# Kernel optimization log

Measured on AMD Instinct MI355X. Metric: run time of the kernel, lower is better.

Reference implementation:

```python
import jax, jax.numpy as jnp
import numpy as np

N = 50000       # nodes
E = 800000      # edges
IN = 64         # input node feature dim
H = 4           # attention heads
C = 32          # per-head channels (h_dim)
HC = H * C      # 128, concat output per conv
ED = 16         # edge feature dim
G = 2000        # number of graphs (molecules)
NEG = 0.2       # GATConv negative slope


def setup_inputs() -> dict:
    key = jax.random.key(0)
    ks = jax.random.split(key, 40)
    rn = lambda k, shp, s=0.1: (jax.random.normal(k, shp, jnp.float32) * s)
    inp = {}
    inp["x"] = jax.random.normal(ks[0], (N, IN), jnp.float32)
    inp["edge_index"] = jax.random.randint(ks[1], (2, E), 0, N)
    inp["edge_attr"] = jax.random.normal(ks[2], (E, ED), jnp.float32)
    inp["batch"] = jnp.sort(jax.random.randint(ks[3], (N,), 0, G))
    dins = [IN, HC, HC]
    i = 4
    for l in (1, 2, 3):
        din = dins[l - 1]
        inp[f"W{l}"] = rn(ks[i], (din, HC)); i += 1
        inp[f"as{l}"] = rn(ks[i], (H, C)); i += 1
        inp[f"ad{l}"] = rn(ks[i], (H, C)); i += 1
        inp[f"We{l}"] = rn(ks[i], (ED, HC)); i += 1
        inp[f"ae{l}"] = rn(ks[i], (H, C)); i += 1
        inp[f"b{l}"] = rn(ks[i], (HC,)); i += 1
    D = 4 * HC
    inp["lw1"] = rn(ks[i], (D, D)); i += 1
    inp["lb1"] = rn(ks[i], (D,)); i += 1
    inp["lw2"] = rn(ks[i], (D, 1)); i += 1
    inp["lb2"] = rn(ks[i], (1,)); i += 1
    return inp


def gat_conv(x, src, dst, edge_attr, W, a_s, a_d, We, a_e, b):
    n = x.shape[0]
    h = (x @ W).reshape(n, H, C)                       # [N,H,C]
    alpha_src = (h * a_s).sum(-1)                      # [N,H]
    alpha_dst = (h * a_d).sum(-1)                      # [N,H]
    he = (edge_attr @ We).reshape(-1, H, C)            # [E,H,C]
    alpha_edge = (he * a_e).sum(-1)                    # [E,H]
    alpha = jax.nn.leaky_relu(alpha_src[src] + alpha_dst[dst] + alpha_edge, NEG)
    # per-destination softmax over incoming edges (stable)
    amax = jax.ops.segment_max(alpha, dst, num_segments=n)
    amax = jnp.where(jnp.isfinite(amax), amax, 0.0)
    ex = jnp.exp(alpha - amax[dst])                    # [E,H]
    denom = jax.ops.segment_sum(ex, dst, num_segments=n)
    w = ex / (denom[dst] + 1e-16)                      # [E,H]
    m = h[src] * w[:, :, None]                         # [E,H,C]
    out = jax.ops.segment_sum(m, dst, num_segments=n)  # [N,H,C]
    return out.reshape(n, HC) + b


def reference(x, edge_index, edge_attr, batch,
              W1, as1, ad1, We1, ae1, b1,
              W2, as2, ad2, We2, ae2, b2,
              W3, as3, ad3, We3, ae3, b3,
              lw1, lb1, lw2, lb2):
    src, dst = edge_index[0], edge_index[1]
    h1 = gat_conv(x, src, dst, edge_attr, W1, as1, ad1, We1, ae1, b1)
    h2 = gat_conv(h1, src, dst, edge_attr, W2, as2, ad2, We2, ae2, b2)
    h3 = gat_conv(h2, src, dst, edge_attr, W3, as3, ad3, We3, ae3, b3)
    h_pool = jax.ops.segment_sum(h3, batch, num_segments=G)  # global_add_pool
    h_pool_ = h_pool[batch]                                  # == repeat_interleave by counts
    h = jnp.concatenate([h1, h2, h3, h_pool_], axis=1)       # [N, 4*HC]
    h = jax.nn.leaky_relu(h @ lw1 + lb1, 0.01)               # torch LeakyReLU default
    return h @ lw2 + lb2                                     # [N, 1]
```

## Files before the change

kernel.cpp:

```cpp
#include <hip/hip_runtime.h>
#include <hip/hip_bf16.h>
#include <math.h>

#define NN 50000
#define NE 800000
#define DIN1 64
#define NHEAD 4
#define CH 32
#define HC 128
#define EDIM 16
#define NG 2000
#define SP 56
#define MAXCH 64
#define MJ 256

typedef __attribute__((ext_vector_type(8))) short short8;
typedef __attribute__((ext_vector_type(4))) float floatx4;

__device__ __forceinline__ float lrelu(float x, float s) { return x > 0.f ? x : s * x; }

__device__ __forceinline__ unsigned short f2bf(float x) {
  unsigned int u = __float_as_uint(x);
  u += 0x7fff + ((u >> 16) & 1);
  return (unsigned short)(u >> 16);
}
__device__ __forceinline__ float bflo(unsigned int u) { return __uint_as_float(u << 16); }
__device__ __forceinline__ float bfhi(unsigned int u) { return __uint_as_float(u & 0xffff0000u); }

__device__ __forceinline__ void async16(void* lds, const void* g) {
  __builtin_amdgcn_global_load_lds((const __attribute__((address_space(1))) unsigned int*)g,
                                   (__attribute__((address_space(3))) unsigned int*)lds, 16, 0, 0);
}

__global__ __launch_bounds__(256) void k_we_a(
    const float* __restrict__ We1, const float* __restrict__ ae1,
    const float* __restrict__ We2, const float* __restrict__ ae2,
    const float* __restrict__ We3, const float* __restrict__ ae3,
    float* __restrict__ we_a) {
  int t = threadIdx.x;
  if (t >= 3 * EDIM * NHEAD) return;
  int l = t / (EDIM * NHEAD);
  int rem = t % (EDIM * NHEAD);
  int d = rem / NHEAD, h = rem % NHEAD;
  const float* We = (l == 0) ? We1 : ((l == 1) ? We2 : We3);
  const float* ae = (l == 0) ? ae1 : ((l == 1) ? ae2 : ae3);
  float s = 0.f;
  for (int c = 0; c < CH; ++c) s += We[d * HC + h * CH + c] * ae[h * CH + c];
  we_a[t] = s;
}

__global__ __launch_bounds__(256) void k_wsd(
    const float* __restrict__ W1, const float* __restrict__ as1, const float* __restrict__ ad1,
    const float* __restrict__ W2, const float* __restrict__ as2, const float* __restrict__ ad2,
    const float* __restrict__ W3, const float* __restrict__ as3, const float* __restrict__ ad3,
    unsigned short* __restrict__ wsdb) {
  int i = blockIdx.x * 256 + threadIdx.x;
  if (i >= 3 * 16 * 128) return;
  int l = i >> 11;
  int col = (i >> 7) & 15;
  int k = i & 127;
  if (col >= 8 || (l == 0 && k >= DIN1)) { wsdb[i] = 0; return; }
  const float* W = (l == 0) ? W1 : ((l == 1) ? W2 : W3);
  int head = col & 3;
  const float* av = (col < 4) ? ((l == 0) ? as1 : ((l == 1) ? as2 : as3))
                              : ((l == 0) ? ad1 : ((l == 1) ? ad2 : ad3));
  float s = 0.f;
  for (int c = 0; c < CH; ++c) s += W[(size_t)k * HC + head * CH + c] * av[head * CH + c];
  wsdb[i] = f2bf(s);
}

__global__ __launch_bounds__(256) void k_lw1t(const float* __restrict__ lw1, unsigned short* __restrict__ lw1tb) {
  int i = blockIdx.x * 256 + threadIdx.x;
  if (i >= 512 * 384) return;
  int n = i / 384, k = i % 384;
  lw1tb[i] = f2bf(lw1[(size_t)k * 512 + n]);
}

__global__ __launch_bounds__(256) void k_wt(const float* __restrict__ W1, const float* __restrict__ W2,
                                            const float* __restrict__ W3, unsigned short* __restrict__ wtb) {
  int i = blockIdx.x * 256 + threadIdx.x;
  if (i < 128 * 64) {
    int j = i / 64, k = i % 64;
    wtb[i] = f2bf(W1[k * HC + j]);
  } else if (i < 128 * 64 + 128 * 128) {
    int ii = i - 128 * 64;
    int j = ii / 128, k = ii % 128;
    wtb[i] = f2bf(W2[k * HC + j]);
  } else if (i < 128 * 64 + 2 * 128 * 128) {
    int ii = i - (128 * 64 + 128 * 128);
    int j = ii / 128, k = ii % 128;
    wtb[i] = f2bf(W3[k * HC + j]);
  }
}

__global__ __launch_bounds__(256) void k_cast(const float* __restrict__ x, unsigned short* __restrict__ xb0) {
  int i = blockIdx.x * 256 + threadIdx.x;
  if (i < NN * DIN1) xb0[i] = f2bf(x[i]);
}

__global__ __launch_bounds__(256) void k_hist(const int* __restrict__ dst, int* __restrict__ cnt) {
  int e = blockIdx.x * 256 + threadIdx.x;
  if (e < NE) atomicAdd(&cnt[dst[e]], 1);
}

__global__ __launch_bounds__(256) void k_scan1(const int* __restrict__ cnt, int* __restrict__ row_start,
                                               int* __restrict__ aux) {
  __shared__ int s[256];
  int t = threadIdx.x;
  int i = blockIdx.x * 256 + t;
  int v = (i < NN) ? cnt[i] : 0;
  s[t] = v;
  __syncthreads();
  for (int off = 1; off < 256; off <<= 1) {
    int tv = (t >= off) ? s[t - off] : 0;
    __syncthreads();
    s[t] += tv;
    __syncthreads();
  }
  if (i < NN) row_start[i] = s[t] - v;
  if (t == 255) aux[blockIdx.x] = s[255];
}

__global__ __launch_bounds__(256) void k_scan2(int* __restrict__ aux, int nb) {
  __shared__ int s[256];
  int t = threadIdx.x;
  int v = (t < nb) ? aux[t] : 0;
  s[t] = v;
  __syncthreads();
  for (int off = 1; off < 256; off <<= 1) {
    int tv = (t >= off) ? s[t - off] : 0;
    __syncthreads();
    s[t] += tv;
    __syncthreads();
  }
  if (t < nb) aux[t] = s[t] - v;
}

__global__ __launch_bounds__(256) void k_scan3(int* __restrict__ row_start, const int* __restrict__ aux) {
  int i = blockIdx.x * 256 + threadIdx.x;
  if (i < NN) row_start[i] += aux[i >> 8];
  else if (i == NN) row_start[NN] = NE;
}

__global__ __launch_bounds__(256) void k_scatter(const int* __restrict__ dst, const int* __restrict__ row_start,
                                                 int* __restrict__ fill, int* __restrict__ perm) {
  int e = blockIdx.x * 256 + threadIdx.x;
  if (e >= NE) return;
  int d = dst[e];
  int p = atomicAdd(&fill[d], 1);
  perm[row_start[d] + p] = e;
}

__global__ __launch_bounds__(256) void k_permute(const int* __restrict__ perm, const int* __restrict__ src,
                                                 const float* __restrict__ edge_attr, const float* __restrict__ wea,
                                                 int* __restrict__ srcp, float* __restrict__ aep) {
  __shared__ float wl[3 * EDIM * NHEAD];
  int t = threadIdx.x;
  if (t < 3 * EDIM * NHEAD) wl[t] = wea[t];
  __syncthreads();
  int pos = blockIdx.x * 256 + t;
  if (pos >= NE) return;
  int e = perm[pos];
  srcp[pos] = src[e];
  float ea[EDIM];
#pragma unroll
  for (int k = 0; k < EDIM; k += 4) {
    float4 v = *(const float4*)&edge_attr[(size_t)e * EDIM + k];
    ea[k] = v.x; ea[k + 1] = v.y; ea[k + 2] = v.z; ea[k + 3] = v.w;
  }
#pragma unroll
  for (int l = 0; l < 3; ++l) {
    float a0 = 0.f, a1 = 0.f, a2 = 0.f, a3 = 0.f;
#pragma unroll
    for (int k = 0; k < EDIM; ++k) {
      float ev = ea[k];
      a0 += ev * wl[l * 64 + k * 4 + 0];
      a1 += ev * wl[l * 64 + k * 4 + 1];
      a2 += ev * wl[l * 64 + k * 4 + 2];
      a3 += ev * wl[l * 64 + k * 4 + 3];
    }
    *(float4*)&aep[(size_t)l * NE * 4 + (size_t)pos * 4] = make_float4(a0, a1, a2, a3);
  }
}

__global__ __launch_bounds__(256) void k_gstart(const int* __restrict__ batch, int* __restrict__ gs) {
  int i = blockIdx.x * 256 + threadIdx.x;
  if (i >= NN) return;
  int b = batch[i];
  if (i == 0) {
    for (int g = 0; g <= b; ++g) gs[g] = 0;
  } else {
    int pb = batch[i - 1];
    for (int g = pb + 1; g <= b; ++g) gs[g] = i;
  }
  if (i == NN - 1) {
    for (int g = b + 1; g <= NG; ++g) gs[g] = NN;
  }
}

template <int K, int ASTRIDE>
__global__ __launch_bounds__(256) void k_conv_mfma(const unsigned short* __restrict__ xin,
                                                   const unsigned short* __restrict__ wt,
                                                   const unsigned short* __restrict__ wsd,
                                                   unsigned short* __restrict__ htb,
                                                   float* __restrict__ asrc, float* __restrict__ adst) {
  __shared__ unsigned short As[128 * SP];
  __shared__ unsigned short Bs[128 * SP];
  __shared__ unsigned short Bs2[16 * SP];
  int t = threadIdx.x;
  int n0 = blockIdx.x * 128;
  int lane = t & 63;
  int wave = t >> 6;
  int wr = wave >> 1, wc = wave & 1;

  floatx4 acc[4][4];
  floatx4 acce[4];
#pragma unroll
  for (int a = 0; a < 4; ++a) {
    acce[a] = (floatx4){0.f, 0.f, 0.f, 0.f};
#pragma unroll
    for (int b = 0; b < 4; ++b) acc[a][b] = (floatx4){0.f, 0.f, 0.f, 0.f};
  }

  int sm = t & 127;
  int sc = (t >> 7) * 16;
  int arow = n0 + sm;
  if (arow >= NN) arow = NN - 1;
  const unsigned short* aglob = xin + (size_t)arow * ASTRIDE + sc;
  const unsigned short* bglob = wt + sm * K + sc;
  unsigned short* asl = As + sm * SP + sc;
  unsigned short* bsl = Bs + sm * SP + sc;

  int frow = lane & 15, fk = (lane >> 4) * 8;
  const unsigned short* arow_p = As + (wr * 64 + frow) * SP + fk;
  const unsigned short* brow_p = Bs + (wc * 64 + frow) * SP + fk;
  const unsigned short* b2row_p = Bs2 + frow * SP + fk;

  for (int k0 = 0; k0 < K; k0 += 32) {
    uint4 a0 = *(const uint4*)(aglob);
    uint4 a1 = *(const uint4*)(aglob + 8);
    uint4 b0 = *(const uint4*)(bglob);
    uint4 b1 = *(const uint4*)(bglob + 8);
    uint4 b2 = make_uint4(0, 0, 0, 0);
    if (t < 64) b2 = *(const uint4*)(wsd + (t >> 2) * 128 + k0 + (t & 3) * 8);
    aglob += 32;
    bglob += 32;
    __syncthreads();
    *(uint4*)(asl) = a0;
    *(uint4*)(asl + 8) = a1;
    *(uint4*)(bsl) = b0;
    *(uint4*)(bsl + 8) = b1;
    if (t < 64) *(uint4*)(Bs2 + (t >> 2) * SP + (t & 3) * 8) = b2;
    __syncthreads();
    short8 af[4], bf[4];
#pragma unroll
    for (int ti = 0; ti < 4; ++ti) af[ti] = *(const short8*)(arow_p + ti * 16 * SP);
#pragma unroll
    for (int tj = 0; tj < 4; ++tj) bf[tj] = *(const short8*)(brow_p + tj * 16 * SP);
#pragma unroll
    for (int ti = 0; ti < 4; ++ti)
#pragma unroll
      for (int tj = 0; tj < 4; ++tj)
        acc[ti][tj] = __builtin_amdgcn_mfma_f32_16x16x32_bf16(af[ti], bf[tj], acc[ti][tj], 0, 0, 0);
    if (wc == 0) {
      short8 bf2 = *(const short8*)(b2row_p);
#pragma unroll
      for (int ti = 0; ti < 4; ++ti)
        acce[ti] = __builtin_amdgcn_mfma_f32_16x16x32_bf16(af[ti], bf2, acce[ti], 0, 0, 0);
    }
    arow_p += 0;
  }

  int q = lane & 15;
  int colg = wc * 64 + q;
#pragma unroll
  for (int ti = 0; ti < 4; ++ti) {
    int rowb = n0 + wr * 64 + ti * 16 + (lane >> 4) * 4;
#pragma unroll
    for (int r = 0; r < 4; ++r) {
      int row = rowb + r;
      if (row < NN) {
        htb[(size_t)row * HC + colg] = f2bf(acc[ti][0][r]);
        htb[(size_t)row * HC + colg + 16] = f2bf(acc[ti][1][r]);
        htb[(size_t)row * HC + colg + 32] = f2bf(acc[ti][2][r]);
        htb[(size_t)row * HC + colg + 48] = f2bf(acc[ti][3][r]);
        if (wc == 0 && q < 8) {
          float v = acce[ti][r];
          if (q < 4) asrc[row * 4 + q] = v;
          else adst[row * 4 + (q - 4)] = v;
        }
      }
    }
  }
}

__global__ __launch_bounds__(256) void k_aggregate(
    const unsigned short* __restrict__ htb, const int* __restrict__ srcp,
    const float* __restrict__ aep, const float* __restrict__ asrc, const float* __restrict__ adst,
    const int* __restrict__ row_start, const float* __restrict__ bias,
    unsigned short* __restrict__ xb, int col0) {
  __shared__ float exs[4][MAXCH][4];
  __shared__ int cns[4];
  int t = threadIdx.x;
  int lane = t & 63, wid = t >> 6;
  int n = blockIdx.x * 4 + wid;
  bool nok = n < NN;
  int rs = nok ? row_start[n] : 0;
  int re = nok ? row_start[n + 1] : 0;
  int deg = re - rs;
  if (lane == 0) cns[wid] = (deg + MAXCH - 1) / MAXCH;
  __syncthreads();
  int maxc = max(max(cns[0], cns[1]), max(cns[2], cns[3]));
  int q = lane & 15, g = lane >> 4;
  int h = q >> 2;
  float4 ad4 = nok ? *(const float4*)&adst[n * 4] : make_float4(0.f, 0.f, 0.f, 0.f);
  float acc[8];
#pragma unroll
  for (int j = 0; j < 8; ++j) acc[j] = 0.f;
  float d0 = 0.f, d1 = 0.f, d2 = 0.f, d3 = 0.f;

  for (int cc = 0; cc < maxc; ++cc) {
    int base = rs + cc * MAXCH;
    int m = re - base;
    if (m > MAXCH) m = MAXCH;
    if (lane < m) {
      int i = base + lane;
      int s = srcp[i];
      float4 ae = *(const float4*)&aep[(size_t)i * 4];
      float4 as4 = *(const float4*)&asrc[s * 4];
      float4 ex;
      ex.x = __expf(lrelu(as4.x + ad4.x + ae.x, 0.2f));
      ex.y = __expf(lrelu(as4.y + ad4.y + ae.y, 0.2f));
      ex.z = __expf(lrelu(as4.z + ad4.z + ae.z, 0.2f));
      ex.w = __expf(lrelu(as4.w + ad4.w + ae.w, 0.2f));
      *(float4*)&exs[wid][lane][0] = ex;
      d0 += ex.x; d1 += ex.y; d2 += ex.z; d3 += ex.w;
    }
    __syncthreads();
    int iters = (m > 0) ? ((m + 7) >> 3) : 0;
    for (int kk = 0; kk < iters; ++kk) {
      int ii0 = kk * 8 + g;
      int ii1 = ii0 + 4;
      int i0 = base + ((ii0 < m) ? ii0 : 0);
      int i1 = base + ((ii1 < m) ? ii1 : 0);
      int s0 = srcp[i0];
      int s1 = srcp[i1];
      uint4 h0 = *(const uint4*)(htb + (size_t)s0 * HC + q * 8);
      uint4 h1 = *(const uint4*)(htb + (size_t)s1 * HC + q * 8);
      float w0 = (ii0 < m) ? exs[wid][ii0][h] : 0.f;
      float w1 = (ii1 < m) ? exs[wid][ii1][h] : 0.f;
      acc[0] += w0 * bflo(h0.x) + w1 * bflo(h1.x);
      acc[1] += w0 * bfhi(h0.x) + w1 * bfhi(h1.x);
      acc[2] += w0 * bflo(h0.y) + w1 * bflo(h1.y);
      acc[3] += w0 * bfhi(h0.y) + w1 * bfhi(h1.y);
      acc[4] += w0 * bflo(h0.z) + w1 * bflo(h1.z);
      acc[5] += w0 * bfhi(h0.z) + w1 * bfhi(h1.z);
      acc[6] += w0 * bflo(h0.w) + w1 * bflo(h1.w);
      acc[7] += w0 * bfhi(h0.w) + w1 * bfhi(h1.w);
    }
    __syncthreads();
  }

#pragma unroll
  for (int mm = 1; mm < 64; mm <<= 1) {
    d0 += __shfl_xor(d0, mm, 64);
    d1 += __shfl_xor(d1, mm, 64);
    d2 += __shfl_xor(d2, mm, 64);
    d3 += __shfl_xor(d3, mm, 64);
  }
#pragma unroll
  for (int j = 0; j < 8; ++j) {
    acc[j] += __shfl_xor(acc[j], 16, 64);
    acc[j] += __shfl_xor(acc[j], 32, 64);
  }
  if (nok && g == 0) {
    float dh = (h == 0) ? d0 : ((h == 1) ? d1 : ((h == 2) ? d2 : d3));
    float inv = 1.f / (dh + 1e-16f);
    unsigned int w[4];
#pragma unroll
    for (int j = 0; j < 4; ++j) {
      float v0 = acc[2 * j] * inv + bias[q * 8 + 2 * j];
      float v1 = acc[2 * j + 1] * inv + bias[q * 8 + 2 * j + 1];
      w[j] = (unsigned int)f2bf(v0) | ((unsigned int)f2bf(v1) << 16);
    }
    *(uint4*)&xb[(size_t)n * 384 + col0 + q * 8] = make_uint4(w[0], w[1], w[2], w[3]);
  }
}

__global__ __launch_bounds__(128) void k_pool(const unsigned short* __restrict__ xb, const int* __restrict__ gs,
                                              float* __restrict__ hpool) {
  int g = blockIdx.x;
  int j = threadIdx.x;
  int s = gs[g], e = gs[g + 1];
  float acc = 0.f;
  for (int i = s; i < e; ++i) acc += bflo((unsigned int)xb[(size_t)i * 384 + 256 + j]);
  hpool[(size_t)g * HC + j] = acc;
}

__global__ __launch_bounds__(256) void k_pool_gemm(const float* __restrict__ hpool, const float* __restrict__ lw1,
                                                   float* __restrict__ ph) {
  __shared__ float hp[16][128];
  int t = threadIdx.x;
  int j0 = blockIdx.x * 128;
  int g0 = blockIdx.y * 16;
  int jj = t & 127, gg = t >> 7;
#pragma unroll
  for (int i = 0; i < 8; ++i) {
    int q = t + 256 * i;
    int row = q >> 7, col = q & 127;
    hp[row][col] = hpool[(size_t)(g0 + row) * HC + col];
  }
  __syncthreads();
  float acc[8];
#pragma unroll
  for (int i = 0; i < 8; ++i) acc[i] = 0.f;
  for (int k = 0; k < HC; ++k) {
    float wv = lw1[(size_t)(384 + k) * 512 + j0 + jj];
#pragma unroll
    for (int gi = 0; gi < 8; ++gi) acc[gi] += hp[gg + 2 * gi][k] * wv;
  }
#pragma unroll
  for (int gi = 0; gi < 8; ++gi) ph[(size_t)(g0 + gg + 2 * gi) * 512 + j0 + jj] = acc[gi];
}

__global__ __launch_bounds__(256) void k_outinit(float* __restrict__ out, const float* __restrict__ lb2) {
  int i = blockIdx.x * 256 + threadIdx.x;
  if (i < NN) out[i] = lb2[0];
}

__global__ __launch_bounds__(256, 2) void k_mlp_mfma(
    const unsigned short* __restrict__ xb, const unsigned short* __restrict__ lw1tb,
    const float* __restrict__ ph, const int* __restrict__ batch,
    const float* __restrict__ lb1, const float* __restrict__ lw2,
    float* __restrict__ out) {
  __shared__ unsigned short As[4 * 128 * 8];
  __shared__ unsigned short Bs[4 * 256 * 8];
  int t = threadIdx.x;
  int j0 = blockIdx.x * MJ;
  int n0 = blockIdx.y * 128;
  int lane = t & 63;
  int wave = t >> 6;
  int wr = wave >> 1, wc = wave & 1;

  floatx4 acc[4][8];
#pragma unroll
  for (int a = 0; a < 4; ++a)
#pragma unroll
    for (int b = 0; b < 8; ++b) acc[a][b] = (floatx4){0.f, 0.f, 0.f, 0.f};

  int arow = n0 + (t & 127);
  if (arow >= NN) arow = NN - 1;
  const unsigned short* agp = xb + (size_t)arow * 384 + (t >> 7) * 8;
  const unsigned short* bgp = lw1tb + (size_t)(j0 + t) * 384;
  unsigned short* asb0 = As + (size_t)(wave * 64) * 8;
  unsigned short* asb1 = As + (size_t)(wave * 64 + 256) * 8;
  unsigned short* bsb[4];
#pragma unroll
  for (int p = 0; p < 4; ++p) bsb[p] = Bs + (size_t)(p * 256 + wave * 64) * 8;

  async16(asb0, agp);
  async16(asb1, agp + 16);
#pragma unroll
  for (int p = 0; p < 4; ++p) async16(bsb[p], bgp + p * 8);

  const unsigned short* afp = As + ((size_t)(lane >> 4) * 128 + wr * 64 + (lane & 15)) * 8;
  const unsigned short* bfp = Bs + ((size_t)(lane >> 4) * 256 + wc * 128 + (lane & 15)) * 8;

  for (int kk = 0; kk < 12; ++kk) {
    __syncthreads();
    short8 af[4], bf[8];
#pragma unroll
    for (int ti = 0; ti < 4; ++ti) af[ti] = *(const short8*)(afp + (size_t)ti * 16 * 8);
#pragma unroll
    for (int tj = 0; tj < 8; ++tj) bf[tj] = *(const short8*)(bfp + (size_t)tj * 16 * 8);
    __syncthreads();
    if (kk < 11) {
      int k0 = (kk + 1) * 32;
      async16(asb0, agp + k0);
      async16(asb1, agp + k0 + 16);
#pragma unroll
      for (int p = 0; p < 4; ++p) async16(bsb[p], bgp + k0 + p * 8);
    }
#pragma unroll
    for (int ti = 0; ti < 4; ++ti)
#pragma unroll
      for (int tj = 0; tj < 8; ++tj)
        acc[ti][tj] = __builtin_amdgcn_mfma_f32_16x16x32_bf16(af[ti], bf[tj], acc[ti][tj], 0, 0, 0);
  }

  int colg = j0 + wc * 128 + (lane & 15);
#pragma unroll
  for (int ti = 0; ti < 4; ++ti) {
    int rowb = n0 + wr * 64 + ti * 16 + (lane >> 4) * 4;
#pragma unroll
    for (int r = 0; r < 4; ++r) {
      int row = rowb + r;
      int rc = (row < NN) ? row : 0;
      int bg = batch[rc];
      float partial = 0.f;
#pragma unroll
      for (int tj = 0; tj < 8; ++tj) {
        int j = colg + tj * 16;
        float v = acc[ti][tj][r] + ph[(size_t)bg * 512 + j] + lb1[j];
        partial += lrelu(v, 0.01f) * lw2[j];
      }
#pragma unroll
      for (int m = 1; m < 16; m <<= 1) partial += __shfl_xor(partial, m, 16);
      if ((lane & 15) == 0 && row < NN) atomicAdd(&out[row], partial);
    }
  }
}

extern "C" void kernel_launch(void* const* d_in, const int* in_sizes, int n_in,
                              void* d_out, int out_size, void* d_ws, size_t ws_size,
                              hipStream_t stream) {
  const float* x = (const float*)d_in[0];
  const int* edge_index = (const int*)d_in[1];
  const int* src = edge_index;
  const int* dstp = edge_index + NE;
  const float* edge_attr = (const float*)d_in[2];
  const int* batch = (const int*)d_in[3];
  const float* W[3] = {(const float*)d_in[4], (const float*)d_in[10], (const float*)d_in[16]};
  const float* as_[3] = {(const float*)d_in[5], (const float*)d_in[11], (const float*)d_in[17]};
  const float* ad_[3] = {(const float*)d_in[6], (const float*)d_in[12], (const float*)d_in[18]};
  const float* We_[3] = {(const float*)d_in[7], (const float*)d_in[13], (const float*)d_in[19]};
  const float* ae_[3] = {(const float*)d_in[8], (const float*)d_in[14], (const float*)d_in[20]};
  const float* b_[3] = {(const float*)d_in[9], (const float*)d_in[15], (const float*)d_in[21]};
  const float* lw1 = (const float*)d_in[22];
  const float* lb1 = (const float*)d_in[23];
  const float* lw2 = (const float*)d_in[24];
  const float* lb2 = (const float*)d_in[25];
  float* out = (float*)d_out;

  float* f = (float*)d_ws;
  size_t o = 0;
  float* asrc = f + o;  o += (size_t)NN * NHEAD;
  float* adst = f + o;  o += (size_t)NN * NHEAD;
  float* wea = f + o;   o += 256;
  float* hpool = f + o; o += (size_t)NG * HC;
  float* ph = f + o;    o += (size_t)NG * 512;
  float* aep = f + o;   o += (size_t)3 * NE * 4;
  unsigned short* xb0 = (unsigned short*)(f + o);   o += (size_t)NN * DIN1 / 2;
  unsigned short* htb = (unsigned short*)(f + o);   o += (size_t)NN * HC / 2;
  unsigned short* xb = (unsigned short*)(f + o);    o += (size_t)NN * 384 / 2;
  unsigned short* wtb = (unsigned short*)(f + o);   o += (size_t)(128 * 64 + 2 * 128 * 128) / 2;
  unsigned short* lw1tb = (unsigned short*)(f + o); o += (512 * 384) / 2;
  unsigned short* wsdb = (unsigned short*)(f + o);  o += (size_t)(3 * 16 * 128) / 2;
  int* row_start = (int*)(f + o);
  int* cnt = row_start + (NN + 1);
  int* fill = cnt + NN;
  int* aux = fill + NN;
  int* gs = aux + 256;
  int* perm = gs + (NG + 1);
  int* srcp = perm + NE;

  const int NB = (NN + 255) / 256;
  const int EB = (NE + 255) / 256;

  hipMemsetAsync(cnt, 0, (size_t)2 * NN * sizeof(int), stream);

  k_we_a<<<1, 256, 0, stream>>>(We_[0], ae_[0], We_[1], ae_[1], We_[2], ae_[2], wea);
  k_wsd<<<(3 * 16 * 128 + 255) / 256, 256, 0, stream>>>(W[0], as_[0], ad_[0], W[1], as_[1], ad_[1],
                                                        W[2], as_[2], ad_[2], wsdb);
  k_lw1t<<<(512 * 384 + 255) / 256, 256, 0, stream>>>(lw1, lw1tb);
  k_wt<<<(128 * 64 + 2 * 128 * 128 + 255) / 256, 256, 0, stream>>>(W[0], W[1], W[2], wtb);
  k_cast<<<(NN * DIN1 + 255) / 256, 256, 0, stream>>>(x, xb0);
  k_hist<<<EB, 256, 0, stream>>>(dstp, cnt);
  k_scan1<<<NB, 256, 0, stream>>>(cnt, row_start, aux);
  k_scan2<<<1, 256, 0, stream>>>(aux, NB);
  k_scan3<<<NB, 256, 0, stream>>>(row_start, aux);
  k_scatter<<<EB, 256, 0, stream>>>(dstp, row_start, fill, perm);
  k_permute<<<EB, 256, 0, stream>>>(perm, src, edge_attr, wea, srcp, aep);
  k_gstart<<<NB, 256, 0, stream>>>(batch, gs);
  k_outinit<<<NB, 256, 0, stream>>>(out, lb2);

  const int CONVB = (NN + 127) / 128;
  unsigned short* wt_l[3] = {wtb, wtb + 128 * 64, wtb + 128 * 64 + 128 * 128};
  for (int l = 0; l < 3; ++l) {
    unsigned short* wsd_l = wsdb + (size_t)l * 16 * 128;
    if (l == 0)
      k_conv_mfma<64, 64><<<CONVB, 256, 0, stream>>>(xb0, wt_l[0], wsd_l, htb, asrc, adst);
    else if (l == 1)
      k_conv_mfma<128, 384><<<CONVB, 256, 0, stream>>>(xb, wt_l[1], wsd_l, htb, asrc, adst);
    else
      k_conv_mfma<128, 384><<<CONVB, 256, 0, stream>>>(xb + 128, wt_l[2], wsd_l, htb, asrc, adst);
    k_aggregate<<<(NN + 3) / 4, 256, 0, stream>>>(htb, srcp, aep + (size_t)l * NE * 4, asrc, adst,
                                                  row_start, b_[l], xb, l * HC);
  }

  k_pool<<<NG, 128, 0, stream>>>(xb, gs, hpool);
  k_pool_gemm<<<dim3(4, NG / 16), 256, 0, stream>>>(hpool, lw1, ph);
  k_mlp_mfma<<<dim3(2, (NN + 127) / 128), 256, 0, stream>>>(xb, lw1tb, ph, batch, lb1, lw2, out);
}
```

Measured before the change: 559.8 us.

## Store activations and weights in k-chunked MFMA-ready layout with async LDS loads

Node features, GEMM weights and the MLP weight matrix are now written in a k-chunk-major layout (8-element chunks by padded row count), so conv and MLP GEMM tiles can be fetched with contiguous 16-byte global_load_lds copies. The conv kernel moves from register-staged, padded-LDS loads to async direct-to-LDS prefetch of the next k-step, overlapping it with the MFMAs. The aggregate, pool and MLP kernels are adapted to read and write the new layout, and the pooling scratch buffer now reuses the layer-0 input buffer. In exchange, pool reads become strided and rows are padded to a multiple of 128.

```diff
diff --git a/kernel.cpp b/kernel.cpp
--- a/kernel.cpp
+++ b/kernel.cpp
@@ -3,6 +3,7 @@
 #include <math.h>
 
 #define NN 50000
+#define NNP 50048
 #define NE 800000
 #define DIN1 64
 #define NHEAD 4
@@ -10,9 +11,7 @@
 #define HC 128
 #define EDIM 16
 #define NG 2000
-#define SP 56
 #define MAXCH 64
-#define MJ 256
 
 typedef __attribute__((ext_vector_type(8))) short short8;
 typedef __attribute__((ext_vector_type(4))) float floatx4;
@@ -59,43 +58,49 @@
   int l = i >> 11;
   int col = (i >> 7) & 15;
   int k = i & 127;
-  if (col >= 8 || (l == 0 && k >= DIN1)) { wsdb[i] = 0; return; }
+  size_t oidx = (size_t)l * 2048 + ((size_t)(k >> 3) * 16 + col) * 8 + (k & 7);
+  if (col >= 8 || (l == 0 && k >= DIN1)) { wsdb[oidx] = 0; return; }
   const float* W = (l == 0) ? W1 : ((l == 1) ? W2 : W3);
   int head = col & 3;
   const float* av = (col < 4) ? ((l == 0) ? as1 : ((l == 1) ? as2 : as3))
                               : ((l == 0) ? ad1 : ((l == 1) ? ad2 : ad3));
   float s = 0.f;
   for (int c = 0; c < CH; ++c) s += W[(size_t)k * HC + head * CH + c] * av[head * CH + c];
-  wsdb[i] = f2bf(s);
-}
-
-__global__ __launch_bounds__(256) void k_lw1t(const float* __restrict__ lw1, unsigned short* __restrict__ lw1tb) {
+  wsdb[oidx] = f2bf(s);
+}
+
+__global__ __launch_bounds__(256) void k_lw1t(const float* __restrict__ lw1, unsigned short* __restrict__ lw1img) {
   int i = blockIdx.x * 256 + threadIdx.x;
   if (i >= 512 * 384) return;
-  int n = i / 384, k = i % 384;
-  lw1tb[i] = f2bf(lw1[(size_t)k * 512 + n]);
+  int j = i / 384, k = i % 384;
+  int jh = j >> 8, jc = j & 255;
+  lw1img[((size_t)jh * 48 * 256 + (size_t)(k >> 3) * 256 + jc) * 8 + (k & 7)] = f2bf(lw1[(size_t)k * 512 + j]);
 }
 
 __global__ __launch_bounds__(256) void k_wt(const float* __restrict__ W1, const float* __restrict__ W2,
                                             const float* __restrict__ W3, unsigned short* __restrict__ wtb) {
   int i = blockIdx.x * 256 + threadIdx.x;
+  if (i >= 128 * 64 + 2 * 128 * 128) return;
+  const float* W;
+  int j, k;
+  size_t base;
   if (i < 128 * 64) {
-    int j = i / 64, k = i % 64;
-    wtb[i] = f2bf(W1[k * HC + j]);
+    W = W1; j = i / 64; k = i % 64; base = 0;
   } else if (i < 128 * 64 + 128 * 128) {
     int ii = i - 128 * 64;
-    int j = ii / 128, k = ii % 128;
-    wtb[i] = f2bf(W2[k * HC + j]);
-  } else if (i < 128 * 64 + 2 * 128 * 128) {
+    W = W2; j = ii / 128; k = ii % 128; base = 8192;
+  } else {
     int ii = i - (128 * 64 + 128 * 128);
-    int j = ii / 128, k = ii % 128;
-    wtb[i] = f2bf(W3[k * HC + j]);
-  }
+    W = W3; j = ii / 128; k = ii % 128; base = 24576;
+  }
+  wtb[base + ((size_t)(k >> 3) * 128 + j) * 8 + (k & 7)] = f2bf(W[(size_t)k * HC + j]);
 }
 
 __global__ __launch_bounds__(256) void k_cast(const float* __restrict__ x, unsigned short* __restrict__ xb0) {
   int i = blockIdx.x * 256 + threadIdx.x;
-  if (i < NN * DIN1) xb0[i] = f2bf(x[i]);
+  if (i >= NN * DIN1) return;
+  int n = i >> 6, k = i & 63;
+  xb0[((size_t)(k >> 3) * NNP + n) * 8 + (k & 7)] = f2bf(x[i]);
 }
 
 __global__ __launch_bounds__(256) void k_hist(const int* __restrict__ dst, int* __restrict__ cnt) {
@@ -198,20 +203,21 @@
   }
 }
 
-template <int K, int ASTRIDE>
+template <int K>
 __global__ __launch_bounds__(256) void k_conv_mfma(const unsigned short* __restrict__ xin,
                                                    const unsigned short* __restrict__ wt,
                                                    const unsigned short* __restrict__ wsd,
                                                    unsigned short* __restrict__ htb,
                                                    float* __restrict__ asrc, float* __restrict__ adst) {
-  __shared__ unsigned short As[128 * SP];
-  __shared__ unsigned short Bs[128 * SP];
-  __shared__ unsigned short Bs2[16 * SP];
+  __shared__ unsigned short As[512 * 8];
+  __shared__ unsigned short Bs[512 * 8];
+  __shared__ unsigned short Bs2[64 * 8];
   int t = threadIdx.x;
   int n0 = blockIdx.x * 128;
   int lane = t & 63;
   int wave = t >> 6;
   int wr = wave >> 1, wc = wave & 1;
+  int kadd = wave >> 1, rb = (wave & 1) * 64;
 
   floatx4 acc[4][4];
   floatx4 acce[4];
@@ -222,53 +228,49 @@
     for (int b = 0; b < 4; ++b) acc[a][b] = (floatx4){0.f, 0.f, 0.f, 0.f};
   }
 
-  int sm = t & 127;
-  int sc = (t >> 7) * 16;
-  int arow = n0 + sm;
-  if (arow >= NN) arow = NN - 1;
-  const unsigned short* aglob = xin + (size_t)arow * ASTRIDE + sc;
-  const unsigned short* bglob = wt + sm * K + sc;
-  unsigned short* asl = As + sm * SP + sc;
-  unsigned short* bsl = Bs + sm * SP + sc;
-
-  int frow = lane & 15, fk = (lane >> 4) * 8;
-  const unsigned short* arow_p = As + (wr * 64 + frow) * SP + fk;
-  const unsigned short* brow_p = Bs + (wc * 64 + frow) * SP + fk;
-  const unsigned short* b2row_p = Bs2 + frow * SP + fk;
-
-  for (int k0 = 0; k0 < K; k0 += 32) {
-    uint4 a0 = *(const uint4*)(aglob);
-    uint4 a1 = *(const uint4*)(aglob + 8);
-    uint4 b0 = *(const uint4*)(bglob);
-    uint4 b1 = *(const uint4*)(bglob + 8);
-    uint4 b2 = make_uint4(0, 0, 0, 0);
-    if (t < 64) b2 = *(const uint4*)(wsd + (t >> 2) * 128 + k0 + (t & 3) * 8);
-    aglob += 32;
-    bglob += 32;
-    __syncthreads();
-    *(uint4*)(asl) = a0;
-    *(uint4*)(asl + 8) = a1;
-    *(uint4*)(bsl) = b0;
-    *(uint4*)(bsl + 8) = b1;
-    if (t < 64) *(uint4*)(Bs2 + (t >> 2) * SP + (t & 3) * 8) = b2;
-    __syncthreads();
-    short8 af[4], bf[4];
-#pragma unroll
-    for (int ti = 0; ti < 4; ++ti) af[ti] = *(const short8*)(arow_p + ti * 16 * SP);
-#pragma unroll
-    for (int tj = 0; tj < 4; ++tj) bf[tj] = *(const short8*)(brow_p + tj * 16 * SP);
+  const unsigned short* afp = As + ((size_t)(lane >> 4) * 128 + wr * 64 + (lane & 15)) * 8;
+  const unsigned short* bfp = Bs + ((size_t)(lane >> 4) * 128 + wc * 64 + (lane & 15)) * 8;
+  const unsigned short* b2fp = Bs2 + ((size_t)(lane >> 4) * 16 + (lane & 15)) * 8;
+
+#pragma unroll
+  for (int p = 0; p < 2; ++p) {
+    async16(As + (size_t)(p * 256 + wave * 64) * 8,
+            xin + ((size_t)(p * 2 + kadd) * NNP + n0 + rb + lane) * 8);
+    async16(Bs + (size_t)(p * 256 + wave * 64) * 8,
+            wt + ((size_t)(p * 2 + kadd) * 128 + rb + lane) * 8);
+  }
+  if (wave == 0) async16(Bs2, wsd + (size_t)lane * 8);
+
+  for (int kk = 0; kk < K / 32; ++kk) {
+    __syncthreads();
+    short8 af[4], bf[4], bf2;
+#pragma unroll
+    for (int ti = 0; ti < 4; ++ti) af[ti] = *(const short8*)(afp + (size_t)ti * 16 * 8);
+#pragma unroll
+    for (int tj = 0; tj < 4; ++tj) bf[tj] = *(const short8*)(bfp + (size_t)tj * 16 * 8);
+    bf2 = *(const short8*)(b2fp);
+    __syncthreads();
+    if (kk < K / 32 - 1) {
+      int kb = (kk + 1) * 4;
+#pragma unroll
+      for (int p = 0; p < 2; ++p) {
+        async16(As + (size_t)(p * 256 + wave * 64) * 8,
+                xin + ((size_t)(kb + p * 2 + kadd) * NNP + n0 + rb + lane) * 8);
+        async16(Bs + (size_t)(p * 256 + wave * 64) * 8,
+                wt + ((size_t)(kb + p * 2 + kadd) * 128 + rb + lane) * 8);
+      }
+      if (wave == 0) async16(Bs2, wsd + ((size_t)kb * 16 + lane) * 8);
+    }
 #pragma unroll
     for (int ti = 0; ti < 4; ++ti)
 #pragma unroll
       for (int tj = 0; tj < 4; ++tj)
         acc[ti][tj] = __builtin_amdgcn_mfma_f32_16x16x32_bf16(af[ti], bf[tj], acc[ti][tj], 0, 0, 0);
     if (wc == 0) {
-      short8 bf2 = *(const short8*)(b2row_p);
 #pragma unroll
       for (int ti = 0; ti < 4; ++ti)
         acce[ti] = __builtin_amdgcn_mfma_f32_16x16x32_bf16(af[ti], bf2, acce[ti], 0, 0, 0);
     }
-    arow_p += 0;
   }
 
   int q = lane & 15;
@@ -298,7 +300,7 @@
     const unsigned short* __restrict__ htb, const int* __restrict__ srcp,
     const float* __restrict__ aep, const float* __restrict__ asrc, const float* __restrict__ adst,
     const int* __restrict__ row_start, const float* __restrict__ bias,
-    unsigned short* __restrict__ xb, int col0) {
+    unsigned short* __restrict__ XBp, int kcoff) {
   __shared__ float exs[4][MAXCH][4];
   __shared__ int cns[4];
   int t = threadIdx.x;
@@ -383,17 +385,18 @@
       float v1 = acc[2 * j + 1] * inv + bias[q * 8 + 2 * j + 1];
       w[j] = (unsigned int)f2bf(v0) | ((unsigned int)f2bf(v1) << 16);
     }
-    *(uint4*)&xb[(size_t)n * 384 + col0 + q * 8] = make_uint4(w[0], w[1], w[2], w[3]);
-  }
-}
-
-__global__ __launch_bounds__(128) void k_pool(const unsigned short* __restrict__ xb, const int* __restrict__ gs,
+    *(uint4*)&XBp[((size_t)(kcoff + q) * NNP + n) * 8] = make_uint4(w[0], w[1], w[2], w[3]);
+  }
+}
+
+__global__ __launch_bounds__(128) void k_pool(const unsigned short* __restrict__ XBp, const int* __restrict__ gs,
                                               float* __restrict__ hpool) {
   int g = blockIdx.x;
   int j = threadIdx.x;
+  int kc = 32 + (j >> 3), sb = j & 7;
   int s = gs[g], e = gs[g + 1];
   float acc = 0.f;
-  for (int i = s; i < e; ++i) acc += bflo((unsigned int)xb[(size_t)i * 384 + 256 + j]);
+  for (int i = s; i < e; ++i) acc += bflo((unsigned int)XBp[((size_t)kc * NNP + i) * 8 + sb]);
   hpool[(size_t)g * HC + j] = acc;
 }
 
@@ -429,43 +432,39 @@
 }
 
 __global__ __launch_bounds__(256, 2) void k_mlp_mfma(
-    const unsigned short* __restrict__ xb, const unsigned short* __restrict__ lw1tb,
+    const unsigned short* __restrict__ XBp, const unsigned short* __restrict__ lw1img,
     const float* __restrict__ ph, const int* __restrict__ batch,
     const float* __restrict__ lb1, const float* __restrict__ lw2,
     float* __restrict__ out) {
-  __shared__ unsigned short As[4 * 128 * 8];
-  __shared__ unsigned short Bs[4 * 256 * 8];
-  int t = threadIdx.x;
-  int j0 = blockIdx.x * MJ;
+  __shared__ unsigned short As[512 * 8];
+  __shared__ unsigned short Bs[1024 * 8];
+  int t = threadIdx.x;
+  int jh = blockIdx.x;
   int n0 = blockIdx.y * 128;
   int lane = t & 63;
   int wave = t >> 6;
   int wr = wave >> 1, wc = wave & 1;
+  int kadd = wave >> 1, rb = (wave & 1) * 64;
+  const unsigned short* bimg = lw1img + (size_t)jh * 48 * 256 * 8;
 
   floatx4 acc[4][8];
 #pragma unroll
   for (int a = 0; a < 4; ++a)
 #pragma unroll
     for (int b = 0; b < 8; ++b) acc[a][b] = (floatx4){0.f, 0.f, 0.f, 0.f};
-
-  int arow = n0 + (t & 127);
-  if (arow >= NN) arow = NN - 1;
-  const unsigned short* agp = xb + (size_t)arow * 384 + (t >> 7) * 8;
-  const unsigned short* bgp = lw1tb + (size_t)(j0 + t) * 384;
-  unsigned short* asb0 = As + (size_t)(wave * 64) * 8;
-  unsigned short* asb1 = As + (size_t)(wave * 64 + 256) * 8;
-  unsigned short* bsb[4];
-#pragma unroll
-  for (int p = 0; p < 4; ++p) bsb[p] = Bs + (size_t)(p * 256 + wave * 64) * 8;
-
-  async16(asb0, agp);
-  async16(asb1, agp + 16);
-#pragma unroll
-  for (int p = 0; p < 4; ++p) async16(bsb[p], bgp + p * 8);
 
   const unsigned short* afp = As + ((size_t)(lane >> 4) * 128 + wr * 64 + (lane & 15)) * 8;
   const unsigned short* bfp = Bs + ((size_t)(lane >> 4) * 256 + wc * 128 + (lane & 15)) * 8;
 
+#pragma unroll
+  for (int p = 0; p < 2; ++p)
+    async16(As + (size_t)(p * 256 + wave * 64) * 8,
+            XBp + ((size_t)(p * 2 + kadd) * NNP + n0 + rb + lane) * 8);
+#pragma unroll
+  for (int p = 0; p < 4; ++p)
+    async16(Bs + (size_t)(p * 256 + wave * 64) * 8,
+            bimg + ((size_t)p * 256 + wave * 64 + lane) * 8);
+
   for (int kk = 0; kk < 12; ++kk) {
     __syncthreads();
     short8 af[4], bf[8];
@@ -475,11 +474,15 @@
     for (int tj = 0; tj < 8; ++tj) bf[tj] = *(const short8*)(bfp + (size_t)tj * 16 * 8);
     __syncthreads();
     if (kk < 11) {
-      int k0 = (kk + 1) * 32;
-      async16(asb0, agp + k0);
-      async16(asb1, agp + k0 + 16);
-#pragma unroll
-      for (int p = 0; p < 4; ++p) async16(bsb[p], bgp + k0 + p * 8);
+      int kb = (kk + 1) * 4;
+#pragma unroll
+      for (int p = 0; p < 2; ++p)
+        async16(As + (size_t)(p * 256 + wave * 64) * 8,
+                XBp + ((size_t)(kb + p * 2 + kadd) * NNP + n0 + rb + lane) * 8);
+#pragma unroll
+      for (int p = 0; p < 4; ++p)
+        async16(Bs + (size_t)(p * 256 + wave * 64) * 8,
+                bimg + ((size_t)(kb + p) * 256 + wave * 64 + lane) * 8);
     }
 #pragma unroll
     for (int ti = 0; ti < 4; ++ti)
@@ -488,7 +491,7 @@
         acc[ti][tj] = __builtin_amdgcn_mfma_f32_16x16x32_bf16(af[ti], bf[tj], acc[ti][tj], 0, 0, 0);
   }
 
-  int colg = j0 + wc * 128 + (lane & 15);
+  int colg = jh * 256 + wc * 128 + (lane & 15);
 #pragma unroll
   for (int ti = 0; ti < 4; ++ti) {
     int rowb = n0 + wr * 64 + ti * 16 + (lane >> 4) * 4;
@@ -538,14 +541,15 @@
   float* adst = f + o;  o += (size_t)NN * NHEAD;
   float* wea = f + o;   o += 256;
   float* hpool = f + o; o += (size_t)NG * HC;
-  float* ph = f + o;    o += (size_t)NG * 512;
   float* aep = f + o;   o += (size_t)3 * NE * 4;
-  unsigned short* xb0 = (unsigned short*)(f + o);   o += (size_t)NN * DIN1 / 2;
+  unsigned short* xb0 = (unsigned short*)(f + o);
+  float* ph = (float*)xb0;
+  o += (size_t)8 * NNP * 8 / 2;
   unsigned short* htb = (unsigned short*)(f + o);   o += (size_t)NN * HC / 2;
-  unsigned short* xb = (unsigned short*)(f + o);    o += (size_t)NN * 384 / 2;
+  unsigned short* XB = (unsigned short*)(f + o);    o += (size_t)48 * NNP * 8 / 2;
   unsigned short* wtb = (unsigned short*)(f + o);   o += (size_t)(128 * 64 + 2 * 128 * 128) / 2;
-  unsigned short* lw1tb = (unsigned short*)(f + o); o += (512 * 384) / 2;
-  unsigned short* wsdb = (unsigned short*)(f + o);  o += (size_t)(3 * 16 * 128) / 2;
+  unsigned short* lw1img = (unsigned short*)(f + o); o += (size_t)2 * 48 * 256 * 8 / 2;
+  unsigned short* wsdb = (unsigned short*)(f + o);  o += (size_t)3 * 2048 / 2;
   int* row_start = (int*)(f + o);
   int* cnt = row_start + (NN + 1);
   int* fill = cnt + NN;
@@ -562,7 +566,7 @@
   k_we_a<<<1, 256, 0, stream>>>(We_[0], ae_[0], We_[1], ae_[1], We_[2], ae_[2], wea);
   k_wsd<<<(3 * 16 * 128 + 255) / 256, 256, 0, stream>>>(W[0], as_[0], ad_[0], W[1], as_[1], ad_[1],
                                                         W[2], as_[2], ad_[2], wsdb);
-  k_lw1t<<<(512 * 384 + 255) / 256, 256, 0, stream>>>(lw1, lw1tb);
+  k_lw1t<<<(512 * 384 + 255) / 256, 256, 0, stream>>>(lw1, lw1img);
   k_wt<<<(128 * 64 + 2 * 128 * 128 + 255) / 256, 256, 0, stream>>>(W[0], W[1], W[2], wtb);
   k_cast<<<(NN * DIN1 + 255) / 256, 256, 0, stream>>>(x, xb0);
   k_hist<<<EB, 256, 0, stream>>>(dstp, cnt);
@@ -574,21 +578,20 @@
   k_gstart<<<NB, 256, 0, stream>>>(batch, gs);
   k_outinit<<<NB, 256, 0, stream>>>(out, lb2);
 
-  const int CONVB = (NN + 127) / 128;
-  unsigned short* wt_l[3] = {wtb, wtb + 128 * 64, wtb + 128 * 64 + 128 * 128};
+  const int CONVB = NNP / 128;
+  unsigned short* wt_l[3] = {wtb, wtb + 8192, wtb + 24576};
   for (int l = 0; l < 3; ++l) {
-    unsigned short* wsd_l = wsdb + (size_t)l * 16 * 128;
+    unsigned short* wsd_l = wsdb + (size_t)l * 2048;
+    const unsigned short* xin = (l == 0) ? xb0 : (XB + (size_t)(l - 1) * 16 * NNP * 8);
     if (l == 0)
-      k_conv_mfma<64, 64><<<CONVB, 256, 0, stream>>>(xb0, wt_l[0], wsd_l, htb, asrc, adst);
-    else if (l == 1)
-      k_conv_mfma<128, 384><<<CONVB, 256, 0, stream>>>(xb, wt_l[1], wsd_l, htb, asrc, adst);
+      k_conv_mfma<64><<<CONVB, 256, 0, stream>>>(xin, wt_l[0], wsd_l, htb, asrc, adst);
     else
-      k_conv_mfma<128, 384><<<CONVB, 256, 0, stream>>>(xb + 128, wt_l[2], wsd_l, htb, asrc, adst);
+      k_conv_mfma<128><<<CONVB, 256, 0, stream>>>(xin, wt_l[l], wsd_l, htb, asrc, adst);
     k_aggregate<<<(NN + 3) / 4, 256, 0, stream>>>(htb, srcp, aep + (size_t)l * NE * 4, asrc, adst,
-                                                  row_start, b_[l], xb, l * HC);
-  }
-
-  k_pool<<<NG, 128, 0, stream>>>(xb, gs, hpool);
+                                                  row_start, b_[l], XB, l * 16);
+  }
+
+  k_pool<<<NG, 128, 0, stream>>>(XB, gs, hpool);
   k_pool_gemm<<<dim3(4, NG / 16), 256, 0, stream>>>(hpool, lw1, ph);
-  k_mlp_mfma<<<dim3(2, (NN + 127) / 128), 256, 0, stream>>>(xb, lw1tb, ph, batch, lb1, lw2, out);
-}
+  k_mlp_mfma<<<dim3(2, NNP / 128), 256, 0, stream>>>(XB, lw1img, ph, batch, lb1, lw2, out);
+}
```

Measured after the change: 520.0 us. 7.1% less time.
